# Kernel optimization log

Measured on AMD Instinct MI355X. Metric: run time of the kernel, lower is better.

Reference implementation:

```python
import jax, jax.numpy as jnp
from jax import lax
import numpy as np

# Quantization / layer config (mirrors QuantizedConv2d init_kwargs)
IN_ZP = 3
OUT_ZP = -2
IN_SCALE = 0.05
OUT_SCALE = 0.1
STRIDE = (1, 1)
PAD = (1, 1)  # (pad_h, pad_w)
DILATION = (1, 1)
GROUPS = 1
FEATURE_BITS = 8
Q_MIN, Q_MAX = -(1 << (FEATURE_BITS - 1)), (1 << (FEATURE_BITS - 1)) - 1  # -128, 127


def setup_inputs() -> dict:
    key = jax.random.key(0)
    k1, k2, k3, k4 = jax.random.split(key, 4)
    N, Cin, H, W = 32, 128, 56, 56
    Cout, KH, KW = 256, 3, 3
    x = jax.random.randint(k1, (N, Cin, H, W), -128, 128, dtype=jnp.int8)
    weight = jax.random.randint(k2, (Cout, Cin, KH, KW), -128, 128, dtype=jnp.int8)
    bias = jax.random.randint(k3, (Cout,), -1000, 1000, dtype=jnp.int32)  # shifted quantized bias
    weight_scale = jax.random.uniform(k4, (Cout,), dtype=jnp.float32, minval=1e-3, maxval=1e-2)
    return {"x": x, "weight": weight, "bias": bias, "weight_scale": weight_scale}


def reference(x, weight, bias, weight_scale):
    # q_y = round((CONV[q_x, q_w] + shifted_bias) * (S_x * S_w / S_y) + Z_y), clamped to int8
    # Pad with the input zero point (NOT zero), matching F.pad(..., value=input_zero_point)
    ph, pw = PAD
    xp = jnp.pad(x, ((0, 0), (0, 0), (ph, ph), (pw, pw)), constant_values=IN_ZP)
    # Exact integer convolution (matches the CPU int32 path; GPU float path rounds
    # back to the same int32 values)
    acc = lax.conv_general_dilated(
        xp.astype(jnp.int32), weight.astype(jnp.int32),
        window_strides=STRIDE, padding='VALID',
        rhs_dilation=DILATION, feature_group_count=GROUPS,
        dimension_numbers=('NCHW', 'OIHW', 'NCHW'))  # [N, Cout, H, W] int32
    acc = acc + bias[None, :, None, None]
    # Fused dequant/requant epilogue: per-channel scale, output zero point, round, clamp
    scale = (IN_SCALE * weight_scale / OUT_SCALE)[None, :, None, None]  # [1, Cout, 1, 1]
    y = acc.astype(jnp.float32) * scale + jnp.float32(OUT_ZP)
    return jnp.clip(jnp.round(y), Q_MIN, Q_MAX).astype(jnp.int8)
```

## Files before the change

kernel.cpp:

```cpp
#include <hip/hip_runtime.h>


#define NB    32
#define CIN   128
#define HH    56
#define WW    56
#define COUT  256
#define HP    58
#define WP    58
#define PIX   (HH*WW)
#define KTOT  1152
#define NCHUNK 18

#define NPT   28
#define BN    112
#define NJ    7
#define PHB1  (NJ*1024)
#define PL    (HP*WP*64)
#define BPB   (2*PL)

typedef int v4i __attribute__((ext_vector_type(4)));

#define GLOAD_LDS(gsrc, ldst) \
    __builtin_amdgcn_global_load_lds( \
        (const __attribute__((address_space(1))) void*)(gsrc), \
        (__attribute__((address_space(3))) void*)(ldst), 16, 0, 0)

__global__ void pack_both_kernel(const int* __restrict__ x,
                                 unsigned char* __restrict__ xp8,
                                 const int* __restrict__ wt,
                                 unsigned char* __restrict__ w8f,
                                 int n0) {
    __shared__ unsigned int lt[WW * 33];
    int bx = blockIdx.x;
    int tid = threadIdx.x;

    if (bx < COUT) {
        int co = bx;
        for (int idx = tid; idx < KTOT/4; idx += 256) {
            int k  = idx * 4;
            int r  = k >> 7;
            int ci = k & 127;
            const int* wb = wt + ((co*CIN + ci)*9 + r);
            int v0 = wb[0], v1 = wb[9], v2 = wb[18], v3 = wb[27];
            unsigned int pack = (v0 & 0xFF) | ((v1 & 0xFF) << 8) |
                                ((v2 & 0xFF) << 16) | ((unsigned)(v3 & 0xFF) << 24);
            int tch = k >> 6;
            size_t dst = ((size_t)((tch*16 + (co >> 4))*16 + (co & 15)))*64 + (k & 63);
            *(unsigned int*)(w8f + dst) = pack;
        }
        return;
    }

    int bxx = bx - COUT;
    int nl = bxx / HP;
    int hp = bxx % HP;
    int nb = n0 + nl;
    unsigned char* slab = xp8 + (size_t)nl * BPB;
    unsigned int* q0 = (unsigned int*)(slab + (size_t)hp * WP * 64);
    unsigned int* q1 = (unsigned int*)(slab + PL + (size_t)hp * WP * 64);

    if (hp == 0 || hp == HP-1) {
        const v4i zp = {0x03030303, 0x03030303, 0x03030303, 0x03030303};
        v4i* a0 = (v4i*)q0;
        v4i* a1 = (v4i*)q1;
        for (int i = tid; i < (WP*64)/16; i += 256) { a0[i] = zp; a1[i] = zp; }
        return;
    }

    int h  = hp - 1;
    int wl = tid & 63;
    int cg = tid >> 6;
    if (wl < WW) {
        const int s = HH*WW;
#pragma unroll
        for (int k = 0; k < 8; ++k) {
            int ci0 = cg*4 + k*16;
            const int* xb = x + (((size_t)(nb*CIN + ci0)*HH + h)*WW + wl);
            int v0 = xb[0], v1 = xb[s], v2 = xb[2*s], v3 = xb[3*s];
            unsigned int pack = (v0 & 0xFF) | ((v1 & 0xFF) << 8) |
                                ((v2 & 0xFF) << 16) | ((unsigned)(v3 & 0xFF) << 24);
            lt[wl*33 + (ci0 >> 2)] = pack;
        }
    }
    __syncthreads();

#pragma unroll
    for (int it = 0; it < 7; ++it) {
        int idx = it*256 + tid;
        int p = idx >> 5;
        int d = idx & 31;
        unsigned int* qq = (d < 16) ? q0 : q1;
        qq[(p + 1)*16 + (d & 15)] = lt[p*33 + d];
    }
    if (tid < 64) {
        int d = tid & 15;
        unsigned int* qq = (tid & 16) ? q1 : q0;
        int col = (tid & 32) ? (WP-1) : 0;
        qq[col*16 + d] = 0x03030303u;
    }
}

__device__ __forceinline__ int koff_of(int t) {
    int r  = t >> 1;
    int kh = (r >= 6) ? 2 : (r >= 3 ? 1 : 0);
    int kw = r - kh*3;
    return (t & 1) * PL + ((kh*WP + kw) << 6);
}

__launch_bounds__(512, 4)
__global__ void conv_kernel(const unsigned char* __restrict__ w8f,
                            const unsigned char* __restrict__ xp8,
                            const int* __restrict__ bias,
                            const float* __restrict__ wscale,
                            int* __restrict__ out,
                            int n0) {
    __shared__ __align__(16) unsigned char ldsB[3*PHB1];

    int nwg = gridDim.x;
    int bx0 = blockIdx.x;
    int q = nwg >> 3, r = nwg & 7;
    int xcd = bx0 & 7, idx8 = bx0 >> 3;
    int bx = (xcd < r ? xcd*(q+1) : r*(q+1) + (xcd-r)*q) + idx8;

    int pt = bx % NPT;
    int nl = bx / NPT;
    int nb = n0 + nl;
    int p0 = pt * BN;

    int tid  = threadIdx.x;
    int lane = tid & 63;
    int wm   = tid >> 6;
    int lr   = lane & 15;
    int lg   = lane >> 4;

    int l4 = lane >> 2;
    int sw = (lane & 3) ^ ((lane >> 3) & 3);
    int slot = (wm < 7) ? wm : 6;
    int slotu = __builtin_amdgcn_readfirstlane(slot);
    int pS = p0 + slot*16 + l4;
    int ph = pS / WW, pw = pS % WW;
    const unsigned char* bsrc =
        xp8 + (size_t)nl*BPB + ((size_t)(ph*WP + pw))*64 + sw*16;

    int rslot = lg ^ ((lr >> 1) & 3);
    int vb = lr*64 + rslot*16;

    const unsigned char* abase =
        w8f + (size_t)(wm*2)*1024 + (lr*64 + lg*16);

    v4i acc[2][NJ];
#pragma unroll
    for (int i = 0; i < 2; ++i)
#pragma unroll
        for (int j = 0; j < NJ; ++j)
            acc[i][j] = (v4i){0, 0, 0, 0};

#define STAGE1(T) \
    GLOAD_LDS(bsrc + koff_of(T), &ldsB[((T)%3)*PHB1 + slotu*1024])

    v4i aA[2], aB[2];
#pragma unroll
    for (int i = 0; i < 2; ++i) aA[i] = *(const v4i*)(abase + i*1024);
    STAGE1(0);

#define ITER(P, AC, ANX) do {                                                  \
        if ((P) < NCHUNK-1) {                                                  \
            _Pragma("unroll")                                                  \
            for (int i_ = 0; i_ < 2; ++i_)                                     \
                ANX[i_] = *(const v4i*)(abase + (size_t)((P)+1)*16384          \
                                        + i_*1024);                            \
            __builtin_amdgcn_sched_barrier(0);                                 \
            STAGE1((P)+1);                                                     \
            asm volatile("s_waitcnt vmcnt(3)" ::: "memory");                   \
        } else {                                                               \
            asm volatile("s_waitcnt vmcnt(0)" ::: "memory");                   \
        }                                                                      \
        __builtin_amdgcn_sched_barrier(0);                                     \
        __builtin_amdgcn_s_barrier();            \
        {                                                                      \
            int roff_ = ((P) % 3) * PHB1;                                      \
            v4i b_[NJ];                                                        \
            _Pragma("unroll")                                                  \
            for (int j_ = 0; j_ < NJ; ++j_)                                    \
                b_[j_] = *(const v4i*)&ldsB[roff_ + vb + j_*1024];             \
            __builtin_amdgcn_s_setprio(1);                                     \
            _Pragma("unroll")                                                  \
            for (int i_ = 0; i_ < 2; ++i_)                                     \
                _Pragma("unroll")                                              \
                for (int j_ = 0; j_ < NJ; ++j_)                                \
                    acc[i_][j_] = __builtin_amdgcn_mfma_i32_16x16x64_i8(       \
                        AC[i_], b_[j_], acc[i_][j_], 0, 0, 0);                 \
            __builtin_amdgcn_s_setprio(0);                                     \
        }                                                                      \
    } while (0)

#pragma unroll
    for (int tt = 0; tt < NCHUNK/2; ++tt) {
        ITER(2*tt,   aA, aB);
        ITER(2*tt+1, aB, aA);
    }
#undef ITER
#undef STAGE1

#pragma unroll
    for (int i = 0; i < 2; ++i) {
#pragma unroll
        for (int rr = 0; rr < 4; ++rr) {
            int co = wm*32 + i*16 + lg*4 + rr;
            float sc = __fdiv_rn(__fmul_rn(0.05f, wscale[co]), 0.1f);
            int bs = bias[co];
            int* orow = out + ((size_t)(nb*COUT + co))*PIX + p0;
#pragma unroll
            for (int j = 0; j < NJ; ++j) {
                float accf = (float)(acc[i][j][rr] + bs);
                float y = __fadd_rn(__fmul_rn(accf, sc), -2.0f);
                y = rintf(y);
                y = fminf(fmaxf(y, -128.0f), 127.0f);
                orow[j*16 + lr] = (int)y;
            }
        }
    }
}

__launch_bounds__(256)
__global__ void conv_direct_kernel(const int* __restrict__ x,
                                   const int* __restrict__ wt,
                                   const int* __restrict__ bias,
                                   const float* __restrict__ wscale,
                                   int* __restrict__ out) {
    size_t idx = (size_t)blockIdx.x * 256 + threadIdx.x;
    if (idx >= (size_t)NB * COUT * PIX) return;
    int w  = idx % WW;
    int h  = (idx / WW) % HH;
    int co = (idx / PIX) % COUT;
    int nb = idx / ((size_t)PIX * COUT);
    int acc = 0;
    for (int ci = 0; ci < CIN; ++ci) {
        const int* xb = x + ((size_t)(nb*CIN + ci)*HH)*WW;
        const int* wb = wt + ((size_t)(co*CIN + ci)*9);
        for (int kh = 0; kh < 3; ++kh) {
            int hh = h + kh - 1;
            for (int kw = 0; kw < 3; ++kw) {
                int ww2 = w + kw - 1;
                int xv = (hh >= 0 && hh < HH && ww2 >= 0 && ww2 < WW)
                         ? xb[hh*WW + ww2] : 3;
                acc += xv * wb[kh*3 + kw];
            }
        }
    }
    float sc = __fdiv_rn(__fmul_rn(0.05f, wscale[co]), 0.1f);
    float y = __fadd_rn(__fmul_rn((float)(acc + bias[co]), sc), -2.0f);
    y = rintf(y);
    y = fminf(fmaxf(y, -128.0f), 127.0f);
    out[idx] = (int)y;
}

extern "C" void kernel_launch(void* const* d_in, const int* in_sizes, int n_in,
                              void* d_out, int out_size, void* d_ws, size_t ws_size,
                              hipStream_t stream) {
    const int*   x      = (const int*)d_in[0];
    const int*   weight = (const int*)d_in[1];
    const int*   bias   = (const int*)d_in[2];
    const float* wscale = (const float*)d_in[3];
    int*         out    = (int*)d_out;

    const size_t XOFF = 320u << 10;
    const size_t SLAB = (size_t)COUT * PIX * 4;

    size_t navail = (ws_size > XOFF) ? (ws_size - XOFF) / BPB : 0;

    unsigned char* w8f = (unsigned char*)d_ws;
    unsigned char* xpw = (unsigned char*)d_ws + XOFF;

    if (navail >= 4) {
        int wsN = (int)(navail < 32 ? navail : 32);
        int Na  = 32 - wsN;
        unsigned char* xpt = (unsigned char*)d_out + (size_t)Na * SLAB;

        if (Na > 0) {
            pack_both_kernel<<<dim3(COUT + Na*HP), dim3(256), 0, stream>>>(
                x, xpt, weight, w8f, 0);
            pack_both_kernel<<<dim3(COUT + wsN*HP), dim3(256), 0, stream>>>(
                x, xpw, weight, w8f, Na);
            conv_kernel<<<dim3(NPT*Na), dim3(512), 0, stream>>>(
                w8f, xpt, bias, wscale, out, 0);
            conv_kernel<<<dim3(NPT*wsN), dim3(512), 0, stream>>>(
                w8f, xpw, bias, wscale, out, Na);
        } else {
            pack_both_kernel<<<dim3(COUT + 32*HP), dim3(256), 0, stream>>>(
                x, xpw, weight, w8f, 0);
            conv_kernel<<<dim3(NPT*32), dim3(512), 0, stream>>>(
                w8f, xpw, bias, wscale, out, 0);
        }
    } else if (navail >= 1) {
        int nchk = navail >= 2 ? 2 : 1;
        for (int n0 = 0; n0 < NB; n0 += nchk) {
            int nc = (NB - n0 < nchk) ? (NB - n0) : nchk;
            pack_both_kernel<<<dim3(COUT + nc*HP), dim3(256), 0, stream>>>(
                x, xpw, weight, w8f, n0);
            conv_kernel<<<dim3(NPT*nc), dim3(512), 0, stream>>>(
                w8f, xpw, bias, wscale, out, n0);
        }
    } else {
        size_t total = (size_t)NB * COUT * PIX;
        conv_direct_kernel<<<dim3((total + 255) / 256), dim3(256), 0, stream>>>(
            x, weight, bias, wscale, out);
    }
}
```

Measured before the change: 56.34 us.

## Software-pipeline LDS B-fragment reads across chunks by deferring part of the MFMAs

Splits each chunk's seven B fragments into a group of four and a group of three. The three-fragment group is read from LDS at the end of one iteration, and its MFMAs run at the start of the next, overlapping the fresh LDS reads. A-fragments now rotate through three register sets so the deferred MFMAs still use the previous chunk's A values, with a tail after the loop for the last chunk. The aim is to hide LDS read latency behind matrix-core work, at the cost of extra VGPR pressure and more explicit waitcnt and sched_barrier ordering.

Result: no change. 57.31 us (+1.7%).

```diff
diff --git a/kernel.cpp b/kernel.cpp
--- a/kernel.cpp
+++ b/kernel.cpp
@@ -160,15 +160,17 @@
     GLOAD_LDS(bsrc + koff_of(T), &ldsB[((T)%3)*PHB1 + slotu*1024])
 
     v4i aA[2], aB[2];
+    v4i bA[4], bB[3];
+
 #pragma unroll
     for (int i = 0; i < 2; ++i) aA[i] = *(const v4i*)(abase + i*1024);
     STAGE1(0);
 
-#define ITER(P, AC, ANX) do {                                                  \
+#define ITER(P, AC, AN) do {                                                   \
         if ((P) < NCHUNK-1) {                                                  \
             _Pragma("unroll")                                                  \
             for (int i_ = 0; i_ < 2; ++i_)                                     \
-                ANX[i_] = *(const v4i*)(abase + (size_t)((P)+1)*16384          \
+                AN[i_] = *(const v4i*)(abase + (size_t)((P)+1)*16384           \
                                         + i_*1024);                            \
             __builtin_amdgcn_sched_barrier(0);                                 \
             STAGE1((P)+1);                                                     \
@@ -180,27 +182,112 @@
         __builtin_amdgcn_s_barrier();            \
         {                                                                      \
             int roff_ = ((P) % 3) * PHB1;                                      \
-            v4i b_[NJ];                                                        \
-            _Pragma("unroll")                                                  \
-            for (int j_ = 0; j_ < NJ; ++j_)                                    \
-                b_[j_] = *(const v4i*)&ldsB[roff_ + vb + j_*1024];             \
+                                         \
+            _Pragma("unroll")                                                  \
+            for (int j_ = 0; j_ < 4; ++j_)                                     \
+                bA[j_] = *(const v4i*)&ldsB[roff_ + vb + j_*1024];             \
+            __builtin_amdgcn_sched_barrier(0);                                 \
+                     \
+            if ((P) > 0) {                                                     \
+                __builtin_amdgcn_s_setprio(1);                                 \
+                _Pragma("unroll")                                              \
+                for (int i_ = 0; i_ < 2; ++i_)                                 \
+                    _Pragma("unroll")                                          \
+                    for (int j_ = 0; j_ < 3; ++j_)                             \
+                        acc[i_][4+j_] = __builtin_amdgcn_mfma_i32_16x16x64_i8( \
+                            AC[i_] ,      \
+                            bB[j_], acc[i_][4+j_], 0, 0, 0);                   \
+                __builtin_amdgcn_s_setprio(0);                                 \
+            }                                                                  \
+            asm volatile("s_waitcnt lgkmcnt(0)" ::: "memory");                 \
+            __builtin_amdgcn_sched_barrier(0);                                 \
             __builtin_amdgcn_s_setprio(1);                                     \
             _Pragma("unroll")                                                  \
             for (int i_ = 0; i_ < 2; ++i_)                                     \
                 _Pragma("unroll")                                              \
-                for (int j_ = 0; j_ < NJ; ++j_)                                \
+                for (int j_ = 0; j_ < 4; ++j_)                                 \
                     acc[i_][j_] = __builtin_amdgcn_mfma_i32_16x16x64_i8(       \
-                        AC[i_], b_[j_], acc[i_][j_], 0, 0, 0);                 \
+                        AC[i_], bA[j_], acc[i_][j_], 0, 0, 0);                 \
             __builtin_amdgcn_s_setprio(0);                                     \
+                          \
+            _Pragma("unroll")                                                  \
+            for (int j_ = 0; j_ < 3; ++j_)                                     \
+                bB[j_] = *(const v4i*)&ldsB[roff_ + vb + (4+j_)*1024];         \
         }                                                                      \
     } while (0)
 
-#pragma unroll
-    for (int tt = 0; tt < NCHUNK/2; ++tt) {
-        ITER(2*tt,   aA, aB);
-        ITER(2*tt+1, aB, aA);
-    }
 #undef ITER
+#define ITER2(P, AC, AP, AN) do {                                              \
+        if ((P) < NCHUNK-1) {                                                  \
+            _Pragma("unroll")                                                  \
+            for (int i_ = 0; i_ < 2; ++i_)                                     \
+                AN[i_] = *(const v4i*)(abase + (size_t)((P)+1)*16384           \
+                                        + i_*1024);                            \
+            __builtin_amdgcn_sched_barrier(0);                                 \
+            STAGE1((P)+1);                                                     \
+            asm volatile("s_waitcnt vmcnt(3)" ::: "memory");                   \
+        } else {                                                               \
+            asm volatile("s_waitcnt vmcnt(0)" ::: "memory");                   \
+        }                                                                      \
+        __builtin_amdgcn_sched_barrier(0);                                     \
+        __builtin_amdgcn_s_barrier();                                          \
+        {                                                                      \
+            int roff_ = ((P) % 3) * PHB1;                                      \
+            _Pragma("unroll")                                                  \
+            for (int j_ = 0; j_ < 4; ++j_)                                     \
+                bA[j_] = *(const v4i*)&ldsB[roff_ + vb + j_*1024];             \
+            __builtin_amdgcn_sched_barrier(0);                                 \
+            if ((P) > 0) {                                                     \
+                __builtin_amdgcn_s_setprio(1);                                 \
+                _Pragma("unroll")                                              \
+                for (int i_ = 0; i_ < 2; ++i_)                                 \
+                    _Pragma("unroll")                                          \
+                    for (int j_ = 0; j_ < 3; ++j_)                             \
+                        acc[i_][4+j_] = __builtin_amdgcn_mfma_i32_16x16x64_i8( \
+                            AP[i_], bB[j_], acc[i_][4+j_], 0, 0, 0);           \
+                __builtin_amdgcn_s_setprio(0);                                 \
+            }                                                                  \
+            asm volatile("s_waitcnt lgkmcnt(0)" ::: "memory");                 \
+            __builtin_amdgcn_sched_barrier(0);                                 \
+            __builtin_amdgcn_s_setprio(1);                                     \
+            _Pragma("unroll")                                                  \
+            for (int i_ = 0; i_ < 2; ++i_)                                     \
+                _Pragma("unroll")                                              \
+                for (int j_ = 0; j_ < 4; ++j_)                                 \
+                    acc[i_][j_] = __builtin_amdgcn_mfma_i32_16x16x64_i8(       \
+                        AC[i_], bA[j_], acc[i_][j_], 0, 0, 0);                 \
+            __builtin_amdgcn_s_setprio(0);                                     \
+            _Pragma("unroll")                                                  \
+            for (int j_ = 0; j_ < 3; ++j_)                                     \
+                bB[j_] = *(const v4i*)&ldsB[roff_ + vb + (4+j_)*1024];         \
+        }                                                                      \
+    } while (0)
+
+    {
+        v4i aC0[2], aC1[2], aC2[2];
+#pragma unroll
+        for (int i = 0; i < 2; ++i) aC0[i] = aA[i];
+
+#define A_OF(P) ((P)%3 == 0 ? aC0 : ((P)%3 == 1 ? aC1 : aC2))
+#pragma unroll
+        for (int p = 0; p < NCHUNK; ++p) {
+            switch (p % 3) {
+            case 0: ITER2(p, aC0, aC2, aC1); break;
+            case 1: ITER2(p, aC1, aC0, aC2); break;
+            case 2: ITER2(p, aC2, aC1, aC0); break;
+            }
+        }
+#undef A_OF
+        asm volatile("s_waitcnt lgkmcnt(0)" ::: "memory");
+        __builtin_amdgcn_sched_barrier(0);
+#pragma unroll
+        for (int i = 0; i < 2; ++i)
+#pragma unroll
+            for (int j = 0; j < 3; ++j)
+                acc[i][4+j] = __builtin_amdgcn_mfma_i32_16x16x64_i8(
+                    aC2[i], bB[j], acc[i][4+j], 0, 0, 0);
+    }
+#undef ITER2
 #undef STAGE1
 
 #pragma unroll
```
